# Optimization experiments

Measured on AMD Instinct MI355X. Metric: run time of the kernel, lower is better.

Reference implementation:

```python
import jax, jax.numpy as jnp
import numpy as np

NUM_PRODUCT = 100000
NUM_USERS = 10000
EMBED_DIM = 512
H = EMBED_DIM // 2          # gru_hidden_size = embedding_dim // 2
MBS = 20                    # max_basket_size
NB = 64                     # baskets per user
K = 256                     # batch of users
B = NB * MBS                # flattened item positions per user
L = 2                       # GRU layers


def setup_inputs() -> dict:
    key = jax.random.key(0)
    ks = jax.random.split(key, 8)
    filter_basket_prob = jax.random.uniform(ks[0], (K, B), dtype=jnp.float32)
    # item ids in [-1, NUM_PRODUCT-1]; -1 is padding (shifted to padding_idx 0)
    input_seq_tensor = jax.random.randint(ks[1], (K, B), 0, NUM_PRODUCT + 1) - 1
    uid = jax.random.randint(ks[2], (K,), 0, NUM_USERS)
    embed_table = 0.02 * jax.random.normal(ks[3], (NUM_PRODUCT + 1, H), dtype=jnp.float32)
    embed_table = embed_table.at[0].set(0.0)  # padding_idx=0
    s = 1.0 / np.sqrt(H)
    w_ih = jax.random.uniform(ks[4], (L, 3 * H, H), jnp.float32, -s, s)
    w_hh = jax.random.uniform(ks[5], (L, 3 * H, H), jnp.float32, -s, s)
    b_ih = jax.random.uniform(ks[6], (L, 3 * H), jnp.float32, -s, s)
    b_hh = jax.random.uniform(ks[7], (L, 3 * H), jnp.float32, -s, s)
    return {"filter_basket_prob": filter_basket_prob, "input_seq_tensor": input_seq_tensor,
            "uid": uid, "embed_table": embed_table,
            "w_ih": w_ih, "w_hh": w_hh, "b_ih": b_ih, "b_hh": b_hh}


def _gru_layer(x, wih, whh, bih, bhh):
    # x: [K, T, H]; torch GRU gate math (r, z, n gate order)
    gi = jnp.einsum('kth,gh->ktg', x, wih) + bih  # [K, T, 3H]

    def step(h, gi_t):
        gh = h @ whh.T + bhh
        ir, iz, inn = jnp.split(gi_t, 3, axis=-1)
        hr, hz, hn = jnp.split(gh, 3, axis=-1)
        r = jax.nn.sigmoid(ir + hr)
        z = jax.nn.sigmoid(iz + hz)
        n = jnp.tanh(inn + r * hn)
        h_new = (1.0 - z) * n + z * h
        return h_new, h_new

    h0 = jnp.zeros((x.shape[0], whh.shape[1]), x.dtype)
    _, hs = jax.lax.scan(step, h0, jnp.swapaxes(gi, 0, 1))  # [T, K, H]
    return jnp.swapaxes(hs, 0, 1)


def reference(filter_basket_prob, input_seq_tensor, uid, embed_table, w_ih, w_hh, b_ih, b_hh):
    Kb, Bb = filter_basket_prob.shape
    Hh = embed_table.shape[1]
    nb = Bb // MBS
    # mask out padding positions (constant w.r.t. grads, as in torch .detach())
    mask = (input_seq_tensor != -1).astype(jnp.float32)
    prob = filter_basket_prob * mask                      # [K, B]
    emb = embed_table[input_seq_tensor + 1]               # [K, B, H]
    emb_f = (emb * prob[..., None]).reshape(Kb, nb, MBS, Hh)
    prob_b = prob.reshape(Kb, nb, MBS)
    filter_b = prob_b.max(axis=-1)                        # [K, NB]
    # avg basket pooling: sum(prob*emb) / (sum(prob) + eps)
    basket_emb = emb_f.sum(axis=2) / (prob_b.sum(axis=-1, keepdims=True) + 1e-10)
    valid = (filter_b > 0).astype(jnp.int32)
    # stable descending sort moves valid baskets to the front, preserving order
    order = jnp.argsort(-valid, axis=-1)                  # [K, NB]
    lengths = valid.sum(axis=-1)
    lengths = lengths + (lengths == 0).astype(lengths.dtype)  # clamp to >= 1
    x = jnp.take_along_axis(basket_emb, order[:, :, None], axis=1)  # [K, NB, H]
    # pack/pad/unsort in the original cancel out: GRU output at t depends only
    # on inputs <= t, so run the full padded scan and read step lengths-1.
    for l in range(w_ih.shape[0]):
        x = _gru_layer(x, w_ih[l], w_hh[l], b_ih[l], b_hh[l])
    return x[jnp.arange(Kb), lengths - 1]                 # [K, H]
```

## Files before the change

kernel.cpp:

```cpp
#include <hip/hip_runtime.h>
#include <cstdint>

#define KU 256
#define NBASK 64
#define MBS 20
#define BITEMS 1280
#define HD 256
#define G3 768
#define TT 64

typedef short v8s __attribute__((ext_vector_type(8)));
typedef float v4f __attribute__((ext_vector_type(4)));
typedef unsigned short v4us __attribute__((ext_vector_type(4)));
typedef unsigned int v4u __attribute__((ext_vector_type(4)));

__device__ __forceinline__ unsigned short f2b(float f){
  uint32_t u = __float_as_uint(f);
  u += 0x7FFFu + ((u >> 16) & 1u);
  return (unsigned short)(u >> 16);
}
__device__ __forceinline__ float b2f(unsigned short s){
  return __uint_as_float(((uint32_t)s) << 16);
}
__device__ __forceinline__ unsigned int packf(float x){
  unsigned short hi = f2b(x);
  unsigned short lo = f2b(x - b2f(hi));
  return ((unsigned int)hi << 16) | lo;
}
__device__ __forceinline__ float unpackf(unsigned int v){
  return b2f((unsigned short)(v >> 16)) + b2f((unsigned short)(v & 0xffffu));
}
__device__ __forceinline__ void waitflag(int* f, int v){
  while (__hip_atomic_load(f, __ATOMIC_ACQUIRE, __HIP_MEMORY_SCOPE_AGENT) < v)
    __builtin_amdgcn_s_sleep(2);
}

__global__ __launch_bounds__(1024) void k_convert(
    const float* __restrict__ wih, const float* __restrict__ whh,
    unsigned short* __restrict__ wih1hi, unsigned short* __restrict__ wih1lo,
    unsigned short* __restrict__ wih2hi, unsigned short* __restrict__ wih2lo,
    unsigned short* __restrict__ whh1hi, unsigned short* __restrict__ whh1lo,
    unsigned short* __restrict__ whh2hi, unsigned short* __restrict__ whh2lo,
    int* __restrict__ flags)
{
  int idx = blockIdx.x * 1024 + threadIdx.x;
  int which = blockIdx.y;
  if (which == 0 && blockIdx.x == 0 && threadIdx.x < 128)
    flags[threadIdx.x] = 0;
  float v;
  if (which == 0)      v = wih[idx];
  else if (which == 1) v = wih[196608 + idx];
  else if (which == 2) v = whh[idx];
  else                 v = whh[196608 + idx];
  unsigned short hi = f2b(v);
  unsigned short lo = f2b(v - b2f(hi));
  if (which == 0)      { wih1hi[idx] = hi; wih1lo[idx] = lo; }
  else if (which == 1) { wih2hi[idx] = hi; wih2lo[idx] = lo; }
  else if (which == 2) { whh1hi[idx] = hi; whh1lo[idx] = lo; }
  else                 { whh2hi[idx] = hi; whh2lo[idx] = lo; }
}

__global__ __launch_bounds__(64) void k_order(
    const float* __restrict__ prob, const int* __restrict__ seq,
    int* __restrict__ order, int* __restrict__ lengths)
{
  int k = blockIdx.x, j = threadIdx.x;
  int base = k * BITEMS + j * MBS;
  float mx = 0.f;
  #pragma unroll
  for (int m = 0; m < MBS; m++) {
    int it = seq[base + m];
    float p = (it >= 0) ? prob[base + m] : 0.f;
    mx = fmaxf(mx, p);
  }
  bool valid = mx > 0.f;
  unsigned long long bal = __ballot(valid);
  int len = __popcll(bal);
  unsigned long long below = bal & ((1ull << j) - 1ull);
  int pos = valid ? __popcll(below) : (len + (j - __popcll(below)));
  order[k * NBASK + j] = pos;
  if (j == 0) lengths[k] = (len > 0) ? len : 1;
}

__global__ __launch_bounds__(256) void k_basket(
    const float* __restrict__ prob, const int* __restrict__ seq,
    const float* __restrict__ table, const int* __restrict__ order,
    unsigned int* __restrict__ xb)
{
  int j = blockIdx.x, k = blockIdx.y;
  int h = threadIdx.x;
  int base = k * BITEMS + j * MBS;
  float acc = 0.f, sp = 0.f;
  #pragma unroll
  for (int m = 0; m < MBS; m++) {
    int it = seq[base + m];
    if (it >= 0) {
      float p = prob[base + m];
      sp += p;
      acc += p * table[(size_t)(it + 1) * HD + h];
    }
  }
  float val = acc / (sp + 1e-10f);
  int dest = order[k * NBASK + j];
  xb[((size_t)k * NBASK + dest) * HD + h] = packf(val);
}

__device__ __forceinline__ void wload_all(
    const unsigned short* __restrict__ w0, const unsigned short* __restrict__ w1,
    const unsigned short* __restrict__ w2, int half4,
    v8s (&cw0)[8], v8s (&cw1)[8], v8s (&cw2)[8])
{
  #pragma unroll
  for (int kk = 0; kk < 8; kk++) {
    int p = (half4 + kk) & 7;
    cw0[kk] = *(const v8s*)(w0 + p * 32);
    cw1[kk] = *(const v8s*)(w1 + p * 32);
    cw2[kk] = *(const v8s*)(w2 + p * 32);
  }
}
template<int K0, int KN>
__device__ __forceinline__ void mfma_run(
    const unsigned short (*h_hi)[256], const unsigned short (*h_lo)[256],
    const unsigned short* __restrict__ nlo_s, int r, int g, int jloc, int half4,
    const v8s (&cw0)[8], const v8s (&cw1)[8], const v8s (&cw2)[8],
    v4f& a0, v4f& a1, v4f& a2)
{
  #pragma unroll
  for (int kk = K0; kk < KN; kk++) {
    int p = (half4 + kk) & 7;
    int slotA = ((p * 4 + g) ^ (r & 7)) * 8;
    v8s ahi = *(const v8s*)&h_hi[r][slotA];
    v8s alo = *(const v8s*)&h_lo[r][slotA];
    v8s nl  = *(const v8s*)&nlo_s[jloc * 256 + slotA];
    a0 = __builtin_amdgcn_mfma_f32_16x16x32_bf16(ahi, cw0[kk], a0, 0, 0, 0);
    a0 = __builtin_amdgcn_mfma_f32_16x16x32_bf16(alo, cw0[kk], a0, 0, 0, 0);
    a1 = __builtin_amdgcn_mfma_f32_16x16x32_bf16(ahi, cw1[kk], a1, 0, 0, 0);
    a1 = __builtin_amdgcn_mfma_f32_16x16x32_bf16(alo, cw1[kk], a1, 0, 0, 0);
    a2 = __builtin_amdgcn_mfma_f32_16x16x32_bf16(ahi, cw2[kk], a2, 0, 0, 0);
    a2 = __builtin_amdgcn_mfma_f32_16x16x32_bf16(alo, cw2[kk], a2, 0, 0, 0);
    a2 = __builtin_amdgcn_mfma_f32_16x16x32_bf16(ahi, nl, a2, 0, 0, 0);
  }
}

__global__ __launch_bounds__(512) void k_pipe(
    const unsigned short* __restrict__ wih1hi, const unsigned short* __restrict__ wih1lo,
    const unsigned short* __restrict__ whh1hi, const unsigned short* __restrict__ whh1lo,
    const unsigned short* __restrict__ wih2hi, const unsigned short* __restrict__ wih2lo,
    const unsigned short* __restrict__ whh2hi, const unsigned short* __restrict__ whh2lo,
    float* __restrict__ gi, unsigned int* __restrict__ pk, unsigned int* __restrict__ h2x,
    const float* __restrict__ bih1, const float* __restrict__ bhh1,
    const float* __restrict__ bih2, const float* __restrict__ bhh2,
    const int* __restrict__ lengths, float* __restrict__ out, int* flags)
{
  __shared__ unsigned short h_hi[16][256], h_lo[16][256];
  __shared__ unsigned short nlo_s[32768];
  int tid = threadIdx.x;
  int l = tid & 63, r = l & 15, g = l >> 4;
  int swv = __builtin_amdgcn_readfirstlane(tid >> 6);
  int bx = blockIdx.x;
  int role = bx >> 5, sub = bx & 31, half = sub >> 4, b = sub & 15;
  int half4 = half * 4;
  int ub = b * 16;
  int jloc = swv * 16 + r, j = half * 128 + jloc;
  int* aflag = flags, *gflag = flags + 32, *bflag = flags + 64, *g1flag = flags + 96;
  int myf = sub, sibf = sub ^ 16;

  const unsigned short* whi_g = (role == 0) ? wih1hi : (role == 1) ? whh1hi
                              : (role == 2) ? wih2hi : whh2hi;
  const unsigned short* wlo_g = (role == 0) ? wih1lo : (role == 1) ? whh1lo
                              : (role == 2) ? wih2lo : whh2lo;
  const float* bb_ = (role == 0) ? bih1 : (role == 1) ? bhh1
                   : (role == 2) ? bih2 : bhh2;

  for (int idx = tid; idx < 4096; idx += 512) {
    ((unsigned short*)h_hi)[idx] = 0;
    ((unsigned short*)h_lo)[idx] = 0;
  }
  const unsigned short* wlo_n = wlo_g + 2 * 65536 + half * 128 * 256;
  for (int idx = tid; idx < 32768; idx += 512) {
    int row = idx >> 8, col = idx & 255;
    int slot = (col >> 3) ^ (row & 7);
    nlo_s[row * 256 + slot * 8 + (col & 7)] = wlo_n[idx];
  }
  const unsigned short* w0 = whi_g + (size_t)j * 256 + g * 8;
  const unsigned short* w1 = w0 + 65536;
  const unsigned short* w2 = w0 + 131072;
  float b_r = bb_[j], b_z = bb_[256 + j], b_n = bb_[512 + j];
  int sibbase = (1 - half) * 128;
  int xu = tid >> 5;
  __syncthreads();

  if (role == 1) {
    float hold[4] = {0.f, 0.f, 0.f, 0.f};
    const unsigned int* gq[4];
    unsigned int* hq[4];
    #pragma unroll
    for (int i = 0; i < 4; i++) {
      gq[i] = (const unsigned int*)gi + (size_t)(ub + g * 4 + i) * TT * G3 + j;
      hq[i] = pk + (size_t)(ub + g * 4 + i) * TT * HD + j;
    }
    for (int t = 0; t < TT; t++) {
      v8s cw0[8], cw1[8], cw2[8];
      wload_all(w0, w1, w2, half4, cw0, cw1, cw2);
      v4f a0 = {0.f,0.f,0.f,0.f}, a1 = {0.f,0.f,0.f,0.f}, a2 = {0.f,0.f,0.f,0.f};
      mfma_run<0,4>(h_hi, h_lo, nlo_s, r, g, jloc, half4, cw0, cw1, cw2, a0, a1, a2);
      if (tid == 0) {
        waitflag(&g1flag[b], t + 1);
        waitflag(&g1flag[16 + b], t + 1);
        if (t > 0) waitflag(&aflag[sibf], t);
      }
      __syncthreads();
      if (t > 0) {
        int sj = sibbase + (tid & 31) * 4;
        v4u pkv = *(const v4u*)&pk[((size_t)(ub + xu) * TT + (t - 1)) * HD + sj];
        int pos = (((sj >> 3) ^ (xu & 7)) << 3) + (sj & 7);
        v4us hv, lv;
        #pragma unroll
        for (int i = 0; i < 4; i++) { hv[i] = (unsigned short)(pkv[i] >> 16); lv[i] = (unsigned short)(pkv[i] & 0xffffu); }
        *(v4us*)&h_hi[xu][pos] = hv;
        *(v4us*)&h_lo[xu][pos] = lv;
      }
      unsigned int vr[4], vz[4], vn[4];
      #pragma unroll
      for (int i = 0; i < 4; i++) {
        vr[i] = gq[i][0]; vz[i] = gq[i][256]; vn[i] = gq[i][512];
        gq[i] += G3;
      }
      __syncthreads();
      mfma_run<4,8>(h_hi, h_lo, nlo_s, r, g, jloc, half4, cw0, cw1, cw2, a0, a1, a2);
      #pragma unroll
      for (int i = 0; i < 4; i++) {
        float hr = a0[i] + b_r, hz = a1[i] + b_z, hn = a2[i] + b_n;
        float rr = 1.f / (1.f + __expf(-(unpackf(vr[i]) + hr)));
        float zz = 1.f / (1.f + __expf(-(unpackf(vz[i]) + hz)));
        float e  = __expf(2.f * (unpackf(vn[i]) + rr * hn));
        float nn = 1.f - 2.f / (e + 1.f);
        float hnew = (1.f - zz) * nn + zz * hold[i];
        hold[i] = hnew;
        unsigned short h_  = f2b(hnew);
        unsigned short lo_ = f2b(hnew - b2f(h_));
        int u = g * 4 + i;
        int pos = (((j >> 3) ^ (u & 7)) << 3) + (j & 7);
        h_hi[u][pos] = h_;
        h_lo[u][pos] = lo_;
        hq[i][0] = ((unsigned int)h_ << 16) | lo_;
        hq[i] += HD;
      }
      __syncthreads();
      if (tid == 0) {
        __threadfence();
        __hip_atomic_store(&aflag[myf], t + 1, __ATOMIC_RELEASE, __HIP_MEMORY_SCOPE_AGENT);
      }
    }
  } else if (role == 3) {
    float hold[4] = {0.f, 0.f, 0.f, 0.f};
    const unsigned int* gq[4];
    int lenr[4];
    #pragma unroll
    for (int i = 0; i < 4; i++) {
      gq[i] = (const unsigned int*)gi + (size_t)(ub + g * 4 + i) * TT * G3 + j;
      lenr[i] = lengths[ub + g * 4 + i];
    }
    for (int t = 0; t < TT; t++) {
      v8s cw0[8], cw1[8], cw2[8];
      wload_all(w0, w1, w2, half4, cw0, cw1, cw2);
      v4f a0 = {0.f,0.f,0.f,0.f}, a1 = {0.f,0.f,0.f,0.f}, a2 = {0.f,0.f,0.f,0.f};
      mfma_run<0,4>(h_hi, h_lo, nlo_s, r, g, jloc, half4, cw0, cw1, cw2, a0, a1, a2);
      if (tid == 0) {
        waitflag(&gflag[myf], t + 1);
        if (t > 0) waitflag(&bflag[sibf], t);
      }
      __syncthreads();
      if (t > 0) {
        int sj = sibbase + (tid & 31) * 4;
        v4u pkv = *(const v4u*)&h2x[((t - 1) & 1) * 65536 + (ub + xu) * HD + sj];
        int pos = (((sj >> 3) ^ (xu & 7)) << 3) + (sj & 7);
        v4us hv, lv;
        #pragma unroll
        for (int i = 0; i < 4; i++) { hv[i] = (unsigned short)(pkv[i] >> 16); lv[i] = (unsigned short)(pkv[i] & 0xffffu); }
        *(v4us*)&h_hi[xu][pos] = hv;
        *(v4us*)&h_lo[xu][pos] = lv;
      }
      unsigned int vr[4], vz[4], vn[4];
      #pragma unroll
      for (int i = 0; i < 4; i++) {
        vr[i] = gq[i][0]; vz[i] = gq[i][256]; vn[i] = gq[i][512];
        gq[i] += G3;
      }
      __syncthreads();
      mfma_run<4,8>(h_hi, h_lo, nlo_s, r, g, jloc, half4, cw0, cw1, cw2, a0, a1, a2);
      #pragma unroll
      for (int i = 0; i < 4; i++) {
        float hr = a0[i] + b_r, hz = a1[i] + b_z, hn = a2[i] + b_n;
        float rr = 1.f / (1.f + __expf(-(unpackf(vr[i]) + hr)));
        float zz = 1.f / (1.f + __expf(-(unpackf(vz[i]) + hz)));
        float e  = __expf(2.f * (unpackf(vn[i]) + rr * hn));
        float nn = 1.f - 2.f / (e + 1.f);
        float hnew = (1.f - zz) * nn + zz * hold[i];
        hold[i] = hnew;
        unsigned short h_  = f2b(hnew);
        unsigned short lo_ = f2b(hnew - b2f(h_));
        int u = g * 4 + i;
        int pos = (((j >> 3) ^ (u & 7)) << 3) + (j & 7);
        h_hi[u][pos] = h_;
        h_lo[u][pos] = lo_;
        h2x[(t & 1) * 65536 + (ub + u) * HD + j] = ((unsigned int)h_ << 16) | lo_;
        if (t == lenr[i] - 1)
          out[(size_t)(ub + u) * HD + j] = hnew;
      }
      __syncthreads();
      if (tid == 0) {
        __threadfence();
        __hip_atomic_store(&bflag[myf], t + 1, __ATOMIC_RELEASE, __HIP_MEMORY_SCOPE_AGENT);
      }
    }
  } else {
    unsigned int* gi_u = (unsigned int*)gi;
    int* postf = (role == 0) ? &g1flag[myf] : &gflag[myf];
    for (int t = 0; t < TT; t++) {
      v8s cw0[8], cw1[8], cw2[8];
      wload_all(w0, w1, w2, half4, cw0, cw1, cw2);
      if (role == 2 && tid == 0) { waitflag(&aflag[b], t + 1); waitflag(&aflag[16 + b], t + 1); }
      __syncthreads();
      {
        int c0 = (tid & 31) * 8;
        const unsigned int* src = &pk[((size_t)(ub + xu) * TT + t) * HD + c0];
        #pragma unroll
        for (int hf = 0; hf < 2; hf++) {
          v4u pkv = *(const v4u*)(src + hf * 4);
          int sj = c0 + hf * 4;
          int pos = (((sj >> 3) ^ (xu & 7)) << 3) + (sj & 7);
          v4us hv, lv;
          #pragma unroll
          for (int i = 0; i < 4; i++) { hv[i] = (unsigned short)(pkv[i] >> 16); lv[i] = (unsigned short)(pkv[i] & 0xffffu); }
          *(v4us*)&h_hi[xu][pos] = hv;
          *(v4us*)&h_lo[xu][pos] = lv;
        }
      }
      __syncthreads();
      v4f a0 = {b_r, b_r, b_r, b_r}, a1 = {b_z, b_z, b_z, b_z}, a2 = {b_n, b_n, b_n, b_n};
      mfma_run<0,8>(h_hi, h_lo, nlo_s, r, g, jloc, half4, cw0, cw1, cw2, a0, a1, a2);
      #pragma unroll
      for (int i = 0; i < 4; i++) {
        size_t base = ((size_t)(ub + g * 4 + i) * TT + t) * G3;
        gi_u[base + j]       = packf(a0[i]);
        gi_u[base + 256 + j] = packf(a1[i]);
        gi_u[base + 512 + j] = packf(a2[i]);
      }
      __syncthreads();
      if (tid == 0) {
        __threadfence();
        __hip_atomic_store(postf, t + 1, __ATOMIC_RELEASE, __HIP_MEMORY_SCOPE_AGENT);
      }
    }
  }
}

extern "C" void kernel_launch(void* const* d_in, const int* in_sizes, int n_in,
                              void* d_out, int out_size, void* d_ws, size_t ws_size,
                              hipStream_t stream) {
  const float* prob  = (const float*)d_in[0];
  const int*   seq   = (const int*)d_in[1];
  const float* table = (const float*)d_in[3];
  const float* wih   = (const float*)d_in[4];
  const float* whh   = (const float*)d_in[5];
  const float* bih   = (const float*)d_in[6];
  const float* bhh   = (const float*)d_in[7];
  float* out = (float*)d_out;

  char* ws = (char*)d_ws;
  float* gi          = (float*)ws;
  unsigned int* pk   = (unsigned int*)(ws + 50331648);
  char* wsw = ws + 67108864;
  const size_t WSZ = 393216;
  unsigned short* wih1hi = (unsigned short*)(wsw + 0 * WSZ);
  unsigned short* wih1lo = (unsigned short*)(wsw + 1 * WSZ);
  unsigned short* wih2hi = (unsigned short*)(wsw + 2 * WSZ);
  unsigned short* wih2lo = (unsigned short*)(wsw + 3 * WSZ);
  unsigned short* whh1hi = (unsigned short*)(wsw + 4 * WSZ);
  unsigned short* whh1lo = (unsigned short*)(wsw + 5 * WSZ);
  unsigned short* whh2hi = (unsigned short*)(wsw + 6 * WSZ);
  unsigned short* whh2lo = (unsigned short*)(wsw + 7 * WSZ);
  int* order   = (int*)(wsw + 8 * WSZ);
  int* lengths = order + KU * NBASK;
  int* flags   = lengths + KU;
  unsigned int* h2x = (unsigned int*)(wsw + 8 * WSZ + 131072);

  k_convert<<<dim3(192, 4), 1024, 0, stream>>>(wih, whh,
      wih1hi, wih1lo, wih2hi, wih2lo, whh1hi, whh1lo, whh2hi, whh2lo, flags);
  k_order<<<dim3(KU), 64, 0, stream>>>(prob, seq, order, lengths);
  k_basket<<<dim3(NBASK, KU), 256, 0, stream>>>(prob, seq, table, order, pk);
  k_pipe<<<dim3(128), 512, 0, stream>>>(
      wih1hi, wih1lo, whh1hi, whh1lo, wih2hi, wih2lo, whh2hi, whh2lo,
      gi, pk, h2x, bih, bhh, bih + G3, bhh + G3, lengths, out, flags);
}
```

Before: 739.4 us.

## Split layer-1 input projection across two block groups by timestep parity

```diff
diff --git a/kernel.cpp b/kernel.cpp
--- a/kernel.cpp
+++ b/kernel.cpp
@@ -45,7 +45,7 @@
 {
   int idx = blockIdx.x * 1024 + threadIdx.x;
   int which = blockIdx.y;
-  if (which == 0 && blockIdx.x == 0 && threadIdx.x < 128)
+  if (which == 0 && blockIdx.x == 0 && threadIdx.x < 160)
     flags[threadIdx.x] = 0;
   float v;
   if (which == 0)      v = wih[idx];
@@ -158,7 +158,10 @@
   int l = tid & 63, r = l & 15, g = l >> 4;
   int swv = __builtin_amdgcn_readfirstlane(tid >> 6);
   int bx = blockIdx.x;
-  int role = bx >> 5, sub = bx & 31, half = sub >> 4, b = sub & 15;
+  int role, sub, tpar = 0;
+  if (bx < 64) { role = 0; sub = bx & 31; tpar = bx >> 5; }
+  else         { role = 1 + ((bx - 64) >> 5); sub = (bx - 64) & 31; }
+  int half = sub >> 4, b = sub & 15;
   int half4 = half * 4;
   int ub = b * 16;
   int jloc = swv * 16 + r, j = half * 128 + jloc;
@@ -205,8 +208,9 @@
       v4f a0 = {0.f,0.f,0.f,0.f}, a1 = {0.f,0.f,0.f,0.f}, a2 = {0.f,0.f,0.f,0.f};
       mfma_run<0,4>(h_hi, h_lo, nlo_s, r, g, jloc, half4, cw0, cw1, cw2, a0, a1, a2);
       if (tid == 0) {
-        waitflag(&g1flag[b], t + 1);
-        waitflag(&g1flag[16 + b], t + 1);
+        int pslot = (t & 1) * 32, pval = (t >> 1) + 1;
+        waitflag(&g1flag[pslot + b], pval);
+        waitflag(&g1flag[pslot + 16 + b], pval);
         if (t > 0) waitflag(&aflag[sibf], t);
       }
       __syncthreads();
@@ -314,13 +318,13 @@
         __hip_atomic_store(&bflag[myf], t + 1, __ATOMIC_RELEASE, __HIP_MEMORY_SCOPE_AGENT);
       }
     }
-  } else {
+  } else if (role == 0) {
     unsigned int* gi_u = (unsigned int*)gi;
-    int* postf = (role == 0) ? &g1flag[myf] : &gflag[myf];
-    for (int t = 0; t < TT; t++) {
+    int* postf = &g1flag[tpar * 32 + myf];
+    for (int tt = 0; tt < TT / 2; tt++) {
+      int t = tt * 2 + tpar;
       v8s cw0[8], cw1[8], cw2[8];
       wload_all(w0, w1, w2, half4, cw0, cw1, cw2);
-      if (role == 2 && tid == 0) { waitflag(&aflag[b], t + 1); waitflag(&aflag[16 + b], t + 1); }
       __syncthreads();
       {
         int c0 = (tid & 31) * 8;
@@ -350,7 +354,45 @@
       __syncthreads();
       if (tid == 0) {
         __threadfence();
-        __hip_atomic_store(postf, t + 1, __ATOMIC_RELEASE, __HIP_MEMORY_SCOPE_AGENT);
+        __hip_atomic_store(postf, tt + 1, __ATOMIC_RELEASE, __HIP_MEMORY_SCOPE_AGENT);
+      }
+    }
+  } else {
+    unsigned int* gi_u = (unsigned int*)gi;
+    for (int t = 0; t < TT; t++) {
+      v8s cw0[8], cw1[8], cw2[8];
+      wload_all(w0, w1, w2, half4, cw0, cw1, cw2);
+      if (tid == 0) { waitflag(&aflag[b], t + 1); waitflag(&aflag[16 + b], t + 1); }
+      __syncthreads();
+      {
+        int c0 = (tid & 31) * 8;
+        const unsigned int* src = &pk[((size_t)(ub + xu) * TT + t) * HD + c0];
+        #pragma unroll
+        for (int hf = 0; hf < 2; hf++) {
+          v4u pkv = *(const v4u*)(src + hf * 4);
+          int sj = c0 + hf * 4;
+          int pos = (((sj >> 3) ^ (xu & 7)) << 3) + (sj & 7);
+          v4us hv, lv;
+          #pragma unroll
+          for (int i = 0; i < 4; i++) { hv[i] = (unsigned short)(pkv[i] >> 16); lv[i] = (unsigned short)(pkv[i] & 0xffffu); }
+          *(v4us*)&h_hi[xu][pos] = hv;
+          *(v4us*)&h_lo[xu][pos] = lv;
+        }
+      }
+      __syncthreads();
+      v4f a0 = {b_r, b_r, b_r, b_r}, a1 = {b_z, b_z, b_z, b_z}, a2 = {b_n, b_n, b_n, b_n};
+      mfma_run<0,8>(h_hi, h_lo, nlo_s, r, g, jloc, half4, cw0, cw1, cw2, a0, a1, a2);
+      #pragma unroll
+      for (int i = 0; i < 4; i++) {
+        size_t base = ((size_t)(ub + g * 4 + i) * TT + t) * G3;
+        gi_u[base + j]       = packf(a0[i]);
+        gi_u[base + 256 + j] = packf(a1[i]);
+        gi_u[base + 512 + j] = packf(a2[i]);
+      }
+      __syncthreads();
+      if (tid == 0) {
+        __threadfence();
+        __hip_atomic_store(&gflag[myf], t + 1, __ATOMIC_RELEASE, __HIP_MEMORY_SCOPE_AGENT);
       }
     }
   }
@@ -390,7 +432,7 @@
       wih1hi, wih1lo, wih2hi, wih2lo, whh1hi, whh1lo, whh2hi, whh2lo, flags);
   k_order<<<dim3(KU), 64, 0, stream>>>(prob, seq, order, lengths);
   k_basket<<<dim3(NBASK, KU), 256, 0, stream>>>(prob, seq, table, order, pk);
-  k_pipe<<<dim3(128), 512, 0, stream>>>(
+  k_pipe<<<dim3(160), 512, 0, stream>>>(
       wih1hi, wih1lo, whh1hi, whh1lo, wih2hi, wih2lo, whh2hi, whh2lo,
       gi, pk, h2x, bih, bhh, bih + G3, bhh + G3, lengths, out, flags);
 }
```

Result: no change. 748.0 us (+1.2%).
